# Kernel optimization log

Measured on AMD Instinct MI355X. Metric: run time of the kernel, lower is better.

The kernel has to match this reference:

```python
import jax, jax.numpy as jnp
import numpy as np

MARGIN = 0.3


def setup_inputs() -> dict:
    key = jax.random.key(0)
    k1, k2 = jax.random.split(key)
    embeddings = jax.random.normal(k1, (128, 512, 1024), dtype=jnp.float32)
    labels = jax.random.randint(k2, (128, 512), 0, 2, dtype=jnp.int64)
    return {"embeddings": embeddings, "labels": labels}


def reference(embeddings, labels):
    # L2-normalize each item embedding (F.normalize, dim=-1)
    emb = embeddings / jnp.linalg.norm(embeddings, axis=-1, keepdims=True)  # [B,N,D]
    dt = emb.dtype

    # Per-sample cosine similarity matrices.
    sim = jnp.einsum('bnd,bmd->bnm', emb, emb)  # [B,N,N]
    diag = jnp.einsum('bnd,bnd->bn', emb, emb)  # [B,N], ~1 after normalization

    pos = labels == 1
    neg = labels == 0
    posf = pos.astype(dt)  # [B,N]
    negf = neg.astype(dt)
    n_pos = pos.sum(-1)  # [B]
    n_neg = neg.sum(-1)

    # Mean similarity of each positive anchor to the OTHER positives
    # (exclude self via diag; original concatenates around p_idx).
    pos_sum = jnp.einsum('bnm,bm->bn', sim, posf) - diag  # [B,N]
    denom_pos = jnp.maximum(n_pos[:, None].astype(dt) - 1, 1)
    pos_sim = jnp.where(n_pos[:, None] > 1, pos_sum / denom_pos, jnp.asarray(1.0, dt))  # [B,N]

    # relu(neg_sim - pos_sim + margin), mean over negatives per anchor.
    tri = jax.nn.relu(sim - pos_sim[:, :, None] + MARGIN)  # [B,N,N]
    denom_neg = jnp.maximum(n_neg[:, None].astype(dt), 1)
    neg_mean = jnp.einsum('bnm,bm->bn', tri, negf) / denom_neg  # [B,N]

    # Only samples with both positives and negatives contribute; one term per positive anchor.
    valid = (n_pos > 0) & (n_neg > 0)  # [B]
    anchor_w = posf * valid[:, None].astype(dt)  # [B,N]
    total = (neg_mean * anchor_w).sum()
    count = (n_pos * valid).sum()
    return total / jnp.maximum(count, 1).astype(dt)
```

## Files before the change

### kernel.cpp

```cpp
#include <hip/hip_runtime.h>
#include <hip/hip_bf16.h>

#define BB 128
#define NN 512
#define DD 1024
#define MARGIN 0.3f

typedef __attribute__((ext_vector_type(8))) short bf16x8;
typedef __attribute__((ext_vector_type(4))) float f32x4;
typedef __attribute__((ext_vector_type(8))) unsigned short ushort8;
typedef long i64f8;

__device__ __forceinline__ unsigned short f2bf(float f) {
    unsigned int u = __float_as_uint(f);
    u += 0x7FFFu + ((u >> 16) & 1u);
    return (unsigned short)(u >> 16);
}
__device__ __forceinline__ int read_label(const unsigned int* lab, int is64, int idx) {
    return (int)(is64 ? lab[2 * idx] : lab[idx]);
}
__device__ __forceinline__ void gload_lds16(const void* g, void* l) {
    __builtin_amdgcn_global_load_lds(
        (const __attribute__((address_space(1))) unsigned int*)g,
        (__attribute__((address_space(3))) unsigned int*)l, 16, 0, 0);
}


__global__ __launch_bounds__(512) void k_compact2(const unsigned int* __restrict__ lab,
                                                  int* __restrict__ slotOf,
                                                  int* __restrict__ counts) {
    int b = blockIdx.x, t = threadIdx.x;
    int lnk = t & 63, wv = t >> 6;

    unsigned int odd = (t < 256) ? lab[2 * (b * 256 + t) + 1] : 0u;
    #pragma unroll
    for (int off = 32; off; off >>= 1) odd |= __shfl_xor(odd, off);
    __shared__ unsigned int ow[8];
    if (lnk == 0) ow[wv] = odd;
    __syncthreads();
    unsigned int tot = ow[0] | ow[1] | ow[2] | ow[3] | ow[4] | ow[5] | ow[6] | ow[7];
    int is64 = (tot == 0) ? 1 : 0;

    int lv = read_label(lab, is64, b * NN + t);
    unsigned long long bp = __ballot(lv == 1);
    int prefP = __popcll(bp & ((1ull << lnk) - 1ull));
    __shared__ int wcP[8];
    if (lnk == 0) wcP[wv] = __popcll(bp);
    __syncthreads();
    int baseP = 0, totP = 0;
    #pragma unroll
    for (int w = 0; w < 8; ++w) {
        int c = wcP[w];
        if (w < wv) baseP += c;
        totP += c;
    }
    int baseN = wv * 64 - baseP;
    int prefN = lnk - prefP;
    int slot = (lv == 1) ? (baseP + prefP) : (totP + baseN + prefN);
    slotOf[b * NN + t] = slot;
    if (t == 0) { counts[2 * b] = totP; counts[2 * b + 1] = NN - totP; }
}

__global__ __launch_bounds__(256) void k_normcvt(const float* __restrict__ x,
                                                 const int* __restrict__ slotOf,
                                                 unsigned char* __restrict__ y8) {
    int wid = blockIdx.x * 4 + (threadIdx.x >> 6);
    int ln = threadIdx.x & 63;
    const f32x4* src = (const f32x4*)(x + (size_t)wid * DD);
    f32x4 v[4];
    float ss = 0.f;
    #pragma unroll
    for (int j = 0; j < 4; ++j) {
        v[j] = __builtin_nontemporal_load(&src[ln + 64 * j]);
        ss += v[j].x * v[j].x + v[j].y * v[j].y + v[j].z * v[j].z + v[j].w * v[j].w;
    }
    #pragma unroll
    for (int off = 32; off; off >>= 1) ss += __shfl_xor(ss, off);
    float r = rsqrtf(ss);
    int b = wid >> 9;
    int slot = slotOf[wid];
    unsigned char* dst = y8 + ((size_t)(b * NN) + slot) * DD;
    #pragma unroll
    for (int j = 0; j < 4; ++j) {
        int w = 0;
        w = __builtin_amdgcn_cvt_pk_fp8_f32(v[j].x * r, v[j].y * r, w, false);
        w = __builtin_amdgcn_cvt_pk_fp8_f32(v[j].z * r, v[j].w * r, w, true);
        *(unsigned int*)&dst[4 * (ln + 64 * j)] = (unsigned int)w;
    }
}

__global__ __launch_bounds__(256) void k_spos2(const unsigned char* __restrict__ y8,
                                               const int* __restrict__ counts,
                                               float* __restrict__ sposPart) {
    int blk = blockIdx.x;
    int b = blk >> 3, sub = blk & 7;
    int t = threadIdx.x, wv = t >> 6, ln = t & 63;
    int P = counts[2 * b];
    int lo = (sub * P) >> 3, hi = ((sub + 1) * P) >> 3;
    const unsigned char* yb = y8 + (size_t)b * NN * DD;
    float acc[16];
    #pragma unroll
    for (int e = 0; e < 16; ++e) acc[e] = 0.f;
    for (int s = lo + wv; s < hi; s += 4) {
        uint4 w = *(const uint4*)(yb + (size_t)s * DD + 16 * ln);
        unsigned int wa[4] = {w.x, w.y, w.z, w.w};
        #pragma unroll
        for (int i = 0; i < 4; ++i) {
            acc[4 * i + 0] += __builtin_amdgcn_cvt_f32_fp8(wa[i], 0);
            acc[4 * i + 1] += __builtin_amdgcn_cvt_f32_fp8(wa[i], 1);
            acc[4 * i + 2] += __builtin_amdgcn_cvt_f32_fp8(wa[i], 2);
            acc[4 * i + 3] += __builtin_amdgcn_cvt_f32_fp8(wa[i], 3);
        }
    }
    __shared__ float part[4][1024];
    #pragma unroll
    for (int i = 0; i < 4; ++i)
        *(float4*)&part[wv][16 * ln + 4 * i] =
            make_float4(acc[4 * i], acc[4 * i + 1], acc[4 * i + 2], acc[4 * i + 3]);
    __syncthreads();
    float* outp = sposPart + (size_t)blk * DD;
    #pragma unroll
    for (int g = 0; g < 4; ++g) {
        int c = t + 256 * g;
        outp[c] = part[0][c] + part[1][c] + part[2][c] + part[3][c];
    }
}

#define TM 128
#define TN 128
#define BKG 64

__global__ __launch_bounds__(256) void k_gemm2(const unsigned char* __restrict__ y8,
                                               const float* __restrict__ sposPart,
                                               const int* __restrict__ counts,
                                               float* __restrict__ partials) {
    int orig = blockIdx.x;
    int blk = (orig & 7) * 256 + (orig >> 3);
    int b = blk >> 4;
    int mt = (blk >> 2) & 3, nt = blk & 3;
    int tid = threadIdx.x;
    int P = counts[2 * b], Q = counts[2 * b + 1];
    if (mt * TM >= P || nt * TN >= Q) {
        if (tid == 0) partials[blk] = 0.f;
        return;
    }

    __shared__ unsigned char As[2 * TM * BKG];
    __shared__ unsigned char Bs[2 * TN * BKG];
    __shared__ unsigned int spos8[DD / 4];
    __shared__ float psA[TM];
    __shared__ float red[4];

    {
        const float* base = sposPart + (size_t)(b * 8) * DD + 4 * tid;
        float4 s = {0.f, 0.f, 0.f, 0.f};
        #pragma unroll
        for (int p = 0; p < 8; ++p) {
            float4 v = *(const float4*)(base + (size_t)p * DD);
            s.x += v.x; s.y += v.y; s.z += v.z; s.w += v.w;
        }
        int w = 0;
        w = __builtin_amdgcn_cvt_pk_fp8_f32(s.x, s.y, w, false);
        w = __builtin_amdgcn_cvt_pk_fp8_f32(s.z, s.w, w, true);
        spos8[tid] = (unsigned int)w;
    }
    asm volatile("s_waitcnt lgkmcnt(0)" ::: "memory");
    __builtin_amdgcn_sched_barrier(0);

    const unsigned char* yb = y8 + (size_t)b * NN * DD;
    int arow0 = mt * TM;
    int brow0 = P + nt * TN;

    int wv = tid >> 6, ln = tid & 63;
    int rr = ln >> 2;
    int sw9s = (rr & 3) ^ ((rr >> 2) & 3);
    int cbS = ((ln & 3) ^ sw9s) * 16;
    int rA[2], rB[2];
    #pragma unroll
    for (int g = 0; g < 2; ++g) {
        rA[g] = arow0 + wv * 32 + g * 16 + rr;
        int rbn = brow0 + wv * 32 + g * 16 + rr;
        rB[g] = (rbn > NN - 1) ? (NN - 1) : rbn;
    }

#define STAGE(bufsel, kk)                                                      \
    {                                                                          \
        _Pragma("unroll")                                                      \
        for (int g_ = 0; g_ < 2; ++g_) {                                       \
            gload_lds16(yb + (size_t)rA[g_] * DD + (kk) + cbS,                 \
                        &As[(bufsel) * TM * BKG + (wv * 32 + g_ * 16) * BKG]); \
            gload_lds16(yb + (size_t)rB[g_] * DD + (kk) + cbS,                 \
                        &Bs[(bufsel) * TN * BKG + (wv * 32 + g_ * 16) * BKG]); \
        }                                                                      \
    }

    int wr = (wv >> 1) * 64, wc = (wv & 1) * 64;
    int fr = ln & 15;
    int swf = (fr & 3) ^ ((fr >> 2) & 3);
    int c0 = ln >> 4;
    bool col0 = (fr == 0);

    f32x4 acc[4][4];
    #pragma unroll
    for (int m = 0; m < 4; ++m)
        #pragma unroll
        for (int n = 0; n < 4; ++n)
            acc[m][n] = (f32x4){0.f, 0.f, 0.f, 0.f};
    f32x4 accE[4];
    #pragma unroll
    for (int m = 0; m < 4; ++m) accE[m] = (f32x4){0.f, 0.f, 0.f, 0.f};

#define COMPUTE(cur, kbase)                                                    \
    {                                                                          \
        i64f8 af[2][4], bfv[2][4], sx[2];                                      \
        _Pragma("unroll")                                                      \
        for (int ks = 0; ks < 2; ++ks) {                                       \
            int cc = c0 + 4 * ks;                                              \
            int off = (((cc >> 1) ^ swf) * 16) + ((cc & 1) * 8);               \
            _Pragma("unroll")                                                  \
            for (int m = 0; m < 4; ++m)                                        \
                af[ks][m] = *(const i64f8*)&As[(cur) * TM * BKG +              \
                                               (wr + m * 16 + fr) * BKG + off];\
            _Pragma("unroll")                                                  \
            for (int n = 0; n < 4; ++n)                                        \
                bfv[ks][n] = *(const i64f8*)&Bs[(cur) * TN * BKG +             \
                                                (wc + n * 16 + fr) * BKG + off];\
            i64f8 sv = *(const i64f8*)&((const unsigned char*)spos8)[(kbase) + \
                                                                     cc * 8];  \
            sx[ks] = col0 ? sv : (i64f8)0;                                     \
        }                                                                      \
        __builtin_amdgcn_s_setprio(1);                                         \
        _Pragma("unroll")                                                      \
        for (int ks = 0; ks < 2; ++ks) {                                       \
            _Pragma("unroll")                                                  \
            for (int m = 0; m < 4; ++m)                                        \
                _Pragma("unroll")                                              \
                for (int n = 0; n < 4; ++n)                                    \
                    acc[m][n] = __builtin_amdgcn_mfma_f32_16x16x32_fp8_fp8(    \
                        af[ks][m], bfv[ks][n], acc[m][n], 0, 0, 0);            \
            _Pragma("unroll")                                                  \
            for (int m = 0; m < 4; ++m)                                        \
                accE[m] = __builtin_amdgcn_mfma_f32_16x16x32_fp8_fp8(          \
                    af[ks][m], sx[ks], accE[m], 0, 0, 0);                      \
        }                                                                      \
        __builtin_amdgcn_s_setprio(0);                                         \
    }

    STAGE(0, 0);
    STAGE(1, BKG);

    for (int t = 0; t < 15; ++t) {
        int cur = t & 1;
        asm volatile("s_waitcnt vmcnt(4)" ::: "memory");
        __builtin_amdgcn_s_barrier();
        __builtin_amdgcn_sched_barrier(0);
        COMPUTE(cur, t * BKG);
        __builtin_amdgcn_s_barrier();
        __builtin_amdgcn_sched_barrier(0);
        if (t < 14) STAGE(cur, (t + 2) * BKG);
    }
    asm volatile("s_waitcnt vmcnt(0)" ::: "memory");
    __builtin_amdgcn_s_barrier();
    __builtin_amdgcn_sched_barrier(0);
    COMPUTE(1, 15 * BKG);
#undef STAGE
#undef COMPUTE

    float invPm1 = (P > 1) ? 1.0f / (float)(P - 1) : 0.f;
    if (col0 && (wv & 1) == 0) {
        int r0 = (ln >> 4) * 4;
        #pragma unroll
        for (int m = 0; m < 4; ++m)
            #pragma unroll
            for (int q = 0; q < 4; ++q)
                psA[wr + m * 16 + r0 + q] =
                    (P > 1) ? (accE[m][q] - 1.0f) * invPm1 : 1.0f;
    }
    __syncthreads();

    float lsum = 0.f;
    int irow0 = wr + (ln >> 4) * 4;
    #pragma unroll
    for (int m = 0; m < 4; ++m) {
        #pragma unroll
        for (int n = 0; n < 4; ++n) {
            int j = wc + fr + n * 16;
            bool jok = (nt * TN + j) < Q;
            #pragma unroll
            for (int q = 0; q < 4; ++q) {
                int i = irow0 + m * 16 + q;
                float v = fmaxf(acc[m][n][q] - psA[i] + MARGIN, 0.f);
                bool iok = (mt * TM + i) < P;
                lsum += (iok && jok) ? v : 0.f;
            }
        }
    }
    #pragma unroll
    for (int off = 32; off; off >>= 1) lsum += __shfl_xor(lsum, off);
    if (ln == 0) red[wv] = lsum;
    __syncthreads();
    if (tid == 0) partials[blk] = (red[0] + red[1] + red[2] + red[3]) / (float)Q;
}

__global__ __launch_bounds__(256) void k_final(const float* __restrict__ partials,
                                               const int* __restrict__ counts,
                                               float* __restrict__ out) {
    int t = threadIdx.x;
    float s = 0.f;
    for (int i = t; i < BB * 16; i += 256) s += partials[i];
    int c = 0;
    for (int b = t; b < BB; b += 256) {
        int P = counts[2 * b], Q = counts[2 * b + 1];
        if (P > 0 && Q > 0) c += P;
    }
    #pragma unroll
    for (int off = 32; off; off >>= 1) {
        s += __shfl_xor(s, off);
        c += __shfl_xor(c, off);
    }
    __shared__ float rs[4];
    __shared__ int ri[4];
    if ((t & 63) == 0) { rs[t >> 6] = s; ri[t >> 6] = c; }
    __syncthreads();
    if (t == 0) {
        float st = rs[0] + rs[1] + rs[2] + rs[3];
        int ct = ri[0] + ri[1] + ri[2] + ri[3];
        out[0] = st / (float)(ct < 1 ? 1 : ct);
    }
}


__global__ __launch_bounds__(256) void k_detect(const unsigned int* __restrict__ lab,
                                                int* __restrict__ flag) {
    int t = threadIdx.x;
    unsigned int acc = 0;
    for (int i = t; i < 32768; i += 256) acc |= lab[2 * i + 1];
    #pragma unroll
    for (int off = 32; off; off >>= 1) acc |= __shfl_xor(acc, off);
    __shared__ unsigned int w[4];
    if ((t & 63) == 0) w[t >> 6] = acc;
    __syncthreads();
    if (t == 0) flag[0] = ((w[0] | w[1] | w[2] | w[3]) == 0) ? 1 : 0;
}

__global__ __launch_bounds__(256) void k_norm_spos(const float* __restrict__ x,
                                                   const unsigned int* __restrict__ lab,
                                                   const int* __restrict__ flag,
                                                   float* __restrict__ rnorm,
                                                   float* __restrict__ sposPart) {
    int blk = blockIdx.x;
    int b = blk >> 2, sub = blk & 3;
    int t = threadIdx.x;
    int m0 = sub * 128;
    __shared__ float rn[128];
    __shared__ int lb[128];
    const float* xb = x + (size_t)b * NN * DD;
    int is64 = flag[0];
    int wv = t >> 6, ln = t & 63;
    for (int r = wv; r < 128; r += 4) {
        const float4* row = (const float4*)(xb + (size_t)(m0 + r) * DD);
        float s = 0.f;
        #pragma unroll
        for (int k = 0; k < 4; ++k) {
            float4 v = row[ln + 64 * k];
            s += v.x * v.x + v.y * v.y + v.z * v.z + v.w * v.w;
        }
        #pragma unroll
        for (int off = 32; off; off >>= 1) s += __shfl_xor(s, off);
        if (ln == 0) {
            float r_ = rsqrtf(s);
            rn[r] = r_;
            rnorm[b * NN + m0 + r] = r_;
        }
    }
    if (t < 128) lb[t] = read_label(lab, is64, b * NN + m0 + t);
    __syncthreads();
    float s0 = 0.f, s1 = 0.f, s2 = 0.f, s3 = 0.f;
    for (int m = 0; m < 128; ++m) {
        if (lb[m] == 1) {
            float rr = rn[m];
            const float* xr = xb + (size_t)(m0 + m) * DD;
            s0 += xr[t] * rr; s1 += xr[t + 256] * rr;
            s2 += xr[t + 512] * rr; s3 += xr[t + 768] * rr;
        }
    }
    float* sp = sposPart + (size_t)blk * DD;
    sp[t] = s0; sp[t + 256] = s1; sp[t + 512] = s2; sp[t + 768] = s3;
}

__global__ __launch_bounds__(512) void k_compact_fb(const unsigned int* __restrict__ lab,
                                                    const int* __restrict__ flag,
                                                    int* __restrict__ posIdx,
                                                    int* __restrict__ negIdx,
                                                    int* __restrict__ counts) {
    int b = blockIdx.x;
    int t = threadIdx.x;
    __shared__ int pidx[NN], nidx[NN];
    __shared__ int cP, cN;
    if (t == 0) { cP = 0; cN = 0; }
    __syncthreads();
    int lv = read_label(lab, flag[0], b * NN + t);
    if (lv == 1)      { int p = atomicAdd(&cP, 1); pidx[p] = t; }
    else if (lv == 0) { int q = atomicAdd(&cN, 1); nidx[q] = t; }
    __syncthreads();
    posIdx[b * NN + t] = (t < cP) ? pidx[t] : 0;
    negIdx[b * NN + t] = (t < cN) ? nidx[t] : 0;
    if (t == 0) { counts[2 * b] = cP; counts[2 * b + 1] = cN; }
}

__global__ __launch_bounds__(256) void k_possim_fb(const float* __restrict__ x,
                                                   const float* __restrict__ rnorm,
                                                   const float* __restrict__ sposPart,
                                                   const int* __restrict__ posIdx,
                                                   const int* __restrict__ counts,
                                                   float* __restrict__ posSimC) {
    int wid = (blockIdx.x * blockDim.x + threadIdx.x) >> 6;
    int ln = threadIdx.x & 63;
    int b = wid >> 9, i = wid & 511;
    int P = counts[2 * b];
    if (i >= P) { if (ln == 0) posSimC[b * NN + i] = 0.f; return; }
    int n = posIdx[b * NN + i];
    const float* xr = x + ((size_t)b * NN + n) * DD;
    const float* sp = sposPart + (size_t)(b * 4) * DD;
    float s = 0.f;
    #pragma unroll
    for (int k = 0; k < 16; ++k) {
        int c = ln + 64 * k;
        float spv = sp[c] + sp[c + DD] + sp[c + 2 * DD] + sp[c + 3 * DD];
        s += xr[c] * spv;
    }
    #pragma unroll
    for (int off = 32; off; off >>= 1) s += __shfl_xor(s, off);
    if (ln == 0) {
        float ps = (P > 1) ? (s * rnorm[b * NN + n] - 1.0f) / (float)(P - 1) : 1.0f;
        posSimC[b * NN + i] = ps;
    }
}

#define LDST 40
#define FTM 128
#define FTN 128
__global__ __launch_bounds__(256) void k_gemm_fb(const float* __restrict__ x,
                                                 const float* __restrict__ rnorm,
                                                 const int* __restrict__ posIdx,
                                                 const int* __restrict__ negIdx,
                                                 const float* __restrict__ posSimC,
                                                 const int* __restrict__ counts,
                                                 float* __restrict__ partials) {
    int blk = blockIdx.x;
    int b = blk >> 4;
    int mt = (blk >> 2) & 3, nt = blk & 3;
    int tid = threadIdx.x;
    int P = counts[2 * b], Q = counts[2 * b + 1];
    if (mt * FTM >= P || nt * FTN >= Q) {
        if (tid == 0) partials[blk] = 0.f;
        return;
    }
    __shared__ unsigned short As[FTM * LDST];
    __shared__ unsigned short Bs[FTN * LDST];
    __shared__ float rnA[FTM], rnB[FTN], psA[FTM];
    __shared__ int gA[FTM], gB[FTN];
    __shared__ float red[4];
    if (tid < FTM) {
        int gi = posIdx[b * NN + mt * FTM + tid];
        gA[tid] = gi;
        rnA[tid] = rnorm[b * NN + gi];
        psA[tid] = posSimC[b * NN + mt * FTM + tid];
    } else {
        int j = tid - FTM;
        int gj = negIdx[b * NN + nt * FTN + j];
        gB[j] = gj;
        rnB[j] = rnorm[b * NN + gj];
    }
    __syncthreads();
    int sr = tid >> 1, sh = tid & 1;
    const float* xb = x + (size_t)b * NN * DD;
    const float* pa = xb + (size_t)gA[sr] * DD + sh * 16;
    const float* pb = xb + (size_t)gB[sr] * DD + sh * 16;
    unsigned short* wa = &As[sr * LDST + sh * 16];
    unsigned short* wb = &Bs[sr * LDST + sh * 16];
    int wv = tid >> 6, ln = tid & 63;
    int wr = (wv >> 1) * 64, wc = (wv & 1) * 64;
    int fr = ln & 15;
    int kh = (ln >> 4) * 8;
    f32x4 acc[4][4];
    #pragma unroll
    for (int m = 0; m < 4; ++m)
        #pragma unroll
        for (int n = 0; n < 4; ++n)
            acc[m][n] = (f32x4){0.f, 0.f, 0.f, 0.f};
    float4 la[4], lbv[4];
    #pragma unroll
    for (int j = 0; j < 4; ++j) {
        la[j]  = *(const float4*)(pa + 4 * j);
        lbv[j] = *(const float4*)(pb + 4 * j);
    }
    for (int k0 = 0; k0 < DD; k0 += 32) {
        ushort8 ua0 = {f2bf(la[0].x), f2bf(la[0].y), f2bf(la[0].z), f2bf(la[0].w),
                       f2bf(la[1].x), f2bf(la[1].y), f2bf(la[1].z), f2bf(la[1].w)};
        ushort8 ua1 = {f2bf(la[2].x), f2bf(la[2].y), f2bf(la[2].z), f2bf(la[2].w),
                       f2bf(la[3].x), f2bf(la[3].y), f2bf(la[3].z), f2bf(la[3].w)};
        ushort8 ub0 = {f2bf(lbv[0].x), f2bf(lbv[0].y), f2bf(lbv[0].z), f2bf(lbv[0].w),
                       f2bf(lbv[1].x), f2bf(lbv[1].y), f2bf(lbv[1].z), f2bf(lbv[1].w)};
        ushort8 ub1 = {f2bf(lbv[2].x), f2bf(lbv[2].y), f2bf(lbv[2].z), f2bf(lbv[2].w),
                       f2bf(lbv[3].x), f2bf(lbv[3].y), f2bf(lbv[3].z), f2bf(lbv[3].w)};
        __syncthreads();
        *(ushort8*)wa = ua0; *(ushort8*)(wa + 8) = ua1;
        *(ushort8*)wb = ub0; *(ushort8*)(wb + 8) = ub1;
        __syncthreads();
        if (k0 + 32 < DD) {
            #pragma unroll
            for (int j = 0; j < 4; ++j) {
                la[j]  = *(const float4*)(pa + k0 + 32 + 4 * j);
                lbv[j] = *(const float4*)(pb + k0 + 32 + 4 * j);
            }
        }
        bf16x8 af[4], bfv[4];
        #pragma unroll
        for (int m = 0; m < 4; ++m)
            af[m] = *(const bf16x8*)&As[(wr + m * 16 + fr) * LDST + kh];
        #pragma unroll
        for (int n = 0; n < 4; ++n)
            bfv[n] = *(const bf16x8*)&Bs[(wc + n * 16 + fr) * LDST + kh];
        #pragma unroll
        for (int m = 0; m < 4; ++m)
            #pragma unroll
            for (int n = 0; n < 4; ++n)
                acc[m][n] = __builtin_amdgcn_mfma_f32_16x16x32_bf16(af[m], bfv[n], acc[m][n], 0, 0, 0);
    }
    float lsum = 0.f;
    int irow0 = wr + (ln >> 4) * 4;
    #pragma unroll
    for (int m = 0; m < 4; ++m) {
        #pragma unroll
        for (int n = 0; n < 4; ++n) {
            int j = wc + fr + n * 16;
            float rbn = rnB[j];
            bool jok = (nt * FTN + j) < Q;
            #pragma unroll
            for (int q = 0; q < 4; ++q) {
                int i = irow0 + m * 16 + q;
                float v = fmaxf(acc[m][n][q] * rnA[i] * rbn - psA[i] + MARGIN, 0.f);
                bool iok = (mt * FTM + i) < P;
                lsum += (iok && jok) ? v : 0.f;
            }
        }
    }
    #pragma unroll
    for (int off = 32; off; off >>= 1) lsum += __shfl_xor(lsum, off);
    if (ln == 0) red[wv] = lsum;
    __syncthreads();
    if (tid == 0) partials[blk] = (red[0] + red[1] + red[2] + red[3]) / (float)Q;
}

__global__ __launch_bounds__(256) void k_final_fb(const float* __restrict__ partials,
                                                  const int* __restrict__ counts,
                                                  float* __restrict__ out) {
    int t = threadIdx.x;
    float s = 0.f;
    for (int i = t; i < BB * 16; i += 256) s += partials[i];
    int c = 0;
    for (int b = t; b < BB; b += 256) {
        int P = counts[2 * b], Q = counts[2 * b + 1];
        if (P > 0 && Q > 0) c += P;
    }
    #pragma unroll
    for (int off = 32; off; off >>= 1) {
        s += __shfl_xor(s, off);
        c += __shfl_xor(c, off);
    }
    __shared__ float rs[4];
    __shared__ int ri[4];
    if ((t & 63) == 0) { rs[t >> 6] = s; ri[t >> 6] = c; }
    __syncthreads();
    if (t == 0) {
        float st = rs[0] + rs[1] + rs[2] + rs[3];
        int ct = ri[0] + ri[1] + ri[2] + ri[3];
        out[0] = st / (float)(ct < 1 ? 1 : ct);
    }
}

extern "C" void kernel_launch(void* const* d_in, const int* in_sizes, int n_in,
                              void* d_out, int out_size, void* d_ws, size_t ws_size,
                              hipStream_t stream) {
    const float* x = (const float*)d_in[0];
    const unsigned int* lab = (const unsigned int*)d_in[1];
    char* ws = (char*)d_ws;
    float* out = (float*)d_out;

    const size_t Y_BYTES = (size_t)BB * NN * DD;
    const size_t O_SLOT  = Y_BYTES;
    const size_t O_CNT   = O_SLOT + 262144;
    const size_t O_SPOS  = O_CNT + 1024;
    const size_t O_PART  = O_SPOS + 4194304;
    const size_t NEED    = O_PART + 16384;

    if (ws_size >= NEED) {
        unsigned char* y8 = (unsigned char*)ws;
        int*   slotOf   = (int*)(ws + O_SLOT);
        int*   counts   = (int*)(ws + O_CNT);
        float* sposPart = (float*)(ws + O_SPOS);
        float* partials = (float*)(ws + O_PART);

        k_compact2<<<BB, 512, 0, stream>>>(lab, slotOf, counts);
        k_normcvt<<<16384, 256, 0, stream>>>(x, slotOf, y8);
        k_spos2<<<BB * 8, 256, 0, stream>>>(y8, counts, sposPart);
        k_gemm2<<<BB * 16, 256, 0, stream>>>(y8, sposPart, counts, partials);
        k_final<<<1, 256, 0, stream>>>(partials, counts, out);
    } else {
        float* rnorm    = (float*)(ws + 0);
        int*   posIdx   = (int*)(ws + 262144);
        int*   negIdx   = (int*)(ws + 524288);
        float* posSimC  = (float*)(ws + 786432);
        float* sposPart = (float*)(ws + 1048576);
        int*   counts   = (int*)(ws + 3145728);
        float* partials = (float*)(ws + 3146752);
        int*   flag     = (int*)(ws + 3154944);

        k_detect<<<1, 256, 0, stream>>>(lab, flag);
        k_norm_spos<<<BB * 4, 256, 0, stream>>>(x, lab, flag, rnorm, sposPart);
        k_compact_fb<<<BB, 512, 0, stream>>>(lab, flag, posIdx, negIdx, counts);
        k_possim_fb<<<16384, 256, 0, stream>>>(x, rnorm, sposPart, posIdx, counts, posSimC);
        k_gemm_fb<<<BB * 16, 256, 0, stream>>>(x, rnorm, posIdx, negIdx, posSimC, counts, partials);
        k_final_fb<<<1, 256, 0, stream>>>(partials, counts, out);
    }
}
```

Measured before the change: 132.2 us.

## Compact GEMM tile list and deepen LDS pipeline to triple buffering

Adds a small kernel that builds a compacted list of non-empty (batch, m-tile, n-tile) work items from the positive/negative counts. The GEMM launches a fixed grid, exits early past the tile count, and reads its tile from the list, so the work is packed densely instead of blocks skipping empty tiles. The K loop also moves from double to triple buffering, with matching vmcnt waits. The cost is one extra launch, more LDS per block (which may reduce occupancy), and dropping the previous XCD-aware block remapping.

Measured after the change: 118.5 us. 10.3% less time.

```diff
diff --git a/kernel.cpp b/kernel.cpp
--- a/kernel.cpp
+++ b/kernel.cpp
@@ -59,6 +59,32 @@
     int slot = (lv == 1) ? (baseP + prefP) : (totP + baseN + prefN);
     slotOf[b * NN + t] = slot;
     if (t == 0) { counts[2 * b] = totP; counts[2 * b + 1] = NN - totP; }
+}
+
+#define TM 128
+#define TN 128
+__global__ __launch_bounds__(128) void k_tiles(const int* __restrict__ counts,
+                                               int* __restrict__ tileList,
+                                               int* __restrict__ nTiles) {
+    int b = threadIdx.x;
+    int P = counts[2 * b], Q = counts[2 * b + 1];
+    int nm = (P > 0) ? (P + TM - 1) / TM : 0;
+    int nn = (Q > 0) ? (Q + TN - 1) / TN : 0;
+    int cnt = nm * nn;
+    __shared__ int pre[128];
+    pre[b] = cnt;
+    __syncthreads();
+    for (int d = 1; d < 128; d <<= 1) {
+        int v = (b >= d) ? pre[b - d] : 0;
+        __syncthreads();
+        pre[b] += v;
+        __syncthreads();
+    }
+    int off = pre[b] - cnt;
+    for (int mt = 0; mt < nm; ++mt)
+        for (int nt = 0; nt < nn; ++nt)
+            tileList[off++] = (b << 8) | (mt << 4) | nt;
+    if (b == 127) nTiles[0] = pre[127];
 }
 
 __global__ __launch_bounds__(256) void k_normcvt(const float* __restrict__ x,
@@ -126,30 +152,28 @@
     }
 }
 
-#define TM 128
-#define TN 128
 #define BKG 64
 
 __global__ __launch_bounds__(256) void k_gemm2(const unsigned char* __restrict__ y8,
                                                const float* __restrict__ sposPart,
                                                const int* __restrict__ counts,
+                                               const int* __restrict__ tileList,
+                                               const int* __restrict__ nTiles,
                                                float* __restrict__ partials) {
-    int orig = blockIdx.x;
-    int blk = (orig & 7) * 256 + (orig >> 3);
-    int b = blk >> 4;
-    int mt = (blk >> 2) & 3, nt = blk & 3;
+    int ticket = blockIdx.x;
+    if (ticket >= nTiles[0]) return;
     int tid = threadIdx.x;
-    int P = counts[2 * b], Q = counts[2 * b + 1];
-    if (mt * TM >= P || nt * TN >= Q) {
-        if (tid == 0) partials[blk] = 0.f;
-        return;
-    }
-
-    __shared__ unsigned char As[2 * TM * BKG];
-    __shared__ unsigned char Bs[2 * TN * BKG];
+    int wv = tid >> 6, ln = tid & 63;
+
+    __shared__ unsigned char As[3 * TM * BKG];
+    __shared__ unsigned char Bs[3 * TN * BKG];
     __shared__ unsigned int spos8[DD / 4];
     __shared__ float psA[TM];
     __shared__ float red[4];
+
+    int desc = tileList[ticket];
+    int b = desc >> 8, mt = (desc >> 4) & 15, nt = desc & 15;
+    int P = counts[2 * b], Q = counts[2 * b + 1];
 
     {
         const float* base = sposPart + (size_t)(b * 8) * DD + 4 * tid;
@@ -171,14 +195,14 @@
     int arow0 = mt * TM;
     int brow0 = P + nt * TN;
 
-    int wv = tid >> 6, ln = tid & 63;
     int rr = ln >> 2;
     int sw9s = (rr & 3) ^ ((rr >> 2) & 3);
     int cbS = ((ln & 3) ^ sw9s) * 16;
     int rA[2], rB[2];
     #pragma unroll
     for (int g = 0; g < 2; ++g) {
-        rA[g] = arow0 + wv * 32 + g * 16 + rr;
+        int ran = arow0 + wv * 32 + g * 16 + rr;
+        rA[g] = (ran > NN - 1) ? (NN - 1) : ran;
         int rbn = brow0 + wv * 32 + g * 16 + rr;
         rB[g] = (rbn > NN - 1) ? (NN - 1) : rbn;
     }
@@ -248,21 +272,21 @@
 
     STAGE(0, 0);
     STAGE(1, BKG);
-
-    for (int t = 0; t < 15; ++t) {
-        int cur = t & 1;
-        asm volatile("s_waitcnt vmcnt(4)" ::: "memory");
+    STAGE(2, 2 * BKG);
+
+    int cur = 0;
+    for (int t = 0; t < 16; ++t) {
+        if (t < 14)       asm volatile("s_waitcnt vmcnt(8)" ::: "memory");
+        else if (t == 14) asm volatile("s_waitcnt vmcnt(4)" ::: "memory");
+        else              asm volatile("s_waitcnt vmcnt(0)" ::: "memory");
         __builtin_amdgcn_s_barrier();
         __builtin_amdgcn_sched_barrier(0);
         COMPUTE(cur, t * BKG);
         __builtin_amdgcn_s_barrier();
         __builtin_amdgcn_sched_barrier(0);
-        if (t < 14) STAGE(cur, (t + 2) * BKG);
-    }
-    asm volatile("s_waitcnt vmcnt(0)" ::: "memory");
-    __builtin_amdgcn_s_barrier();
-    __builtin_amdgcn_sched_barrier(0);
-    COMPUTE(1, 15 * BKG);
+        if (t < 13) STAGE(cur, (t + 3) * BKG);
+        cur = (cur == 2) ? 0 : cur + 1;
+    }
 #undef STAGE
 #undef COMPUTE
 
@@ -299,15 +323,17 @@
     for (int off = 32; off; off >>= 1) lsum += __shfl_xor(lsum, off);
     if (ln == 0) red[wv] = lsum;
     __syncthreads();
-    if (tid == 0) partials[blk] = (red[0] + red[1] + red[2] + red[3]) / (float)Q;
+    if (tid == 0) partials[ticket] = (red[0] + red[1] + red[2] + red[3]) / (float)Q;
 }
 
 __global__ __launch_bounds__(256) void k_final(const float* __restrict__ partials,
+                                               const int* __restrict__ nTiles,
                                                const int* __restrict__ counts,
                                                float* __restrict__ out) {
     int t = threadIdx.x;
+    int A = nTiles[0];
     float s = 0.f;
-    for (int i = t; i < BB * 16; i += 256) s += partials[i];
+    for (int i = t; i < A; i += 256) s += partials[i];
     int c = 0;
     for (int b = t; b < BB; b += 256) {
         int P = counts[2 * b], Q = counts[2 * b + 1];
@@ -593,7 +619,9 @@
     const size_t O_CNT   = O_SLOT + 262144;
     const size_t O_SPOS  = O_CNT + 1024;
     const size_t O_PART  = O_SPOS + 4194304;
-    const size_t NEED    = O_PART + 16384;
+    const size_t O_TILE  = O_PART + 16384;
+    const size_t O_NT    = O_TILE + 8192;
+    const size_t NEED    = O_NT + 64;
 
     if (ws_size >= NEED) {
         unsigned char* y8 = (unsigned char*)ws;
@@ -601,12 +629,15 @@
         int*   counts   = (int*)(ws + O_CNT);
         float* sposPart = (float*)(ws + O_SPOS);
         float* partials = (float*)(ws + O_PART);
+        int*   tileList = (int*)(ws + O_TILE);
+        int*   nTiles   = (int*)(ws + O_NT);
 
         k_compact2<<<BB, 512, 0, stream>>>(lab, slotOf, counts);
+        k_tiles<<<1, 128, 0, stream>>>(counts, tileList, nTiles);
         k_normcvt<<<16384, 256, 0, stream>>>(x, slotOf, y8);
         k_spos2<<<BB * 8, 256, 0, stream>>>(y8, counts, sposPart);
-        k_gemm2<<<BB * 16, 256, 0, stream>>>(y8, sposPart, counts, partials);
-        k_final<<<1, 256, 0, stream>>>(partials, counts, out);
+        k_gemm2<<<2048, 256, 0, stream>>>(y8, sposPart, counts, tileList, nTiles, partials);
+        k_final<<<1, 256, 0, stream>>>(partials, nTiles, counts, out);
     } else {
         float* rnorm    = (float*)(ws + 0);
         int*   posIdx   = (int*)(ws + 262144);
```
